# Kernel optimization log

Hardware: AMD Instinct MI355X
Metric: run time of the kernel (lower is better)

## Reference

```python
import jax, jax.numpy as jnp
import numpy as np
from jax import lax

B, T, D, NH = 8, 2048, 128, 4
HD = D // NH
EPS = 1e-5


def _ln(x, g, b):
    m = x.mean(-1, keepdims=True)
    v = ((x - m) ** 2).mean(-1, keepdims=True)
    return (x - m) / jnp.sqrt(v + EPS) * g + b


def _gelu(x):  # exact (erf) GELU, matching torch nn.GELU default
    return jax.nn.gelu(x, approximate=False)


def _forward(lob_feat, trade_feat, has_trade,
             ei_w, ei_b, ei_g, ei_beta, decay,
             in_proj_w, in_proj_b, out_proj_w, out_proj_b,
             cn_g, cn_b,
             lob_w, lob_b, lob_g, lob_beta,
             tr_w, tr_b, tr_g, tr_beta,
             of_w, of_b, of_g, of_beta):
    # event impact: Linear -> LayerNorm -> Tanh, gated by has_trade
    impact = jnp.tanh(_ln(trade_feat @ ei_w.T + ei_b, ei_g, ei_beta))
    impact = impact * has_trade[..., None]              # [B,T,D]

    # diagonal linear recurrence: state_t = sigmoid(decay) * state_{t-1} + impact_t
    d = jax.nn.sigmoid(decay)                           # [D]

    def step(s, x):
        s = d * s + x
        return s, s

    _, states = lax.scan(step, jnp.zeros_like(impact[:, 0]),
                         jnp.swapaxes(impact, 0, 1))    # [T,B,D]
    state_seq = jnp.swapaxes(states, 0, 1)              # [B,T,D]

    # fusion MLPs (dropout is identity in eval)
    lob_enh = _gelu(_ln(jnp.concatenate([lob_feat, state_seq], -1) @ lob_w.T + lob_b,
                        lob_g, lob_beta))
    trade_enh = _gelu(_ln(jnp.concatenate([trade_feat, state_seq], -1) @ tr_w.T + tr_b,
                          tr_g, tr_beta))

    # torch nn.MultiheadAttention (batch_first): q=lob_enh, k=v=trade_enh
    wq, wk, wv = in_proj_w[:D], in_proj_w[D:2 * D], in_proj_w[2 * D:]
    bq, bk, bv = in_proj_b[:D], in_proj_b[D:2 * D], in_proj_b[2 * D:]
    q = (lob_enh @ wq.T + bq).reshape(B, T, NH, HD)
    k = (trade_enh @ wk.T + bk).reshape(B, T, NH, HD)
    v = (trade_enh @ wv.T + bv).reshape(B, T, NH, HD)
    scores = jnp.einsum('bqhd,bkhd->bhqk', q, k) / jnp.sqrt(jnp.float32(HD))
    attn = jax.nn.softmax(scores, axis=-1)
    ctx = jnp.einsum('bhqk,bkhd->bqhd', attn, v).reshape(B, T, D)
    fused_attn = ctx @ out_proj_w.T + out_proj_b

    fused = _ln(lob_enh + fused_attn, cn_g, cn_b)
    output = _gelu(_ln(jnp.concatenate([fused, trade_enh], -1) @ of_w.T + of_b,
                       of_g, of_beta))
    return output


def setup_inputs() -> dict:
    key = jax.random.key(0)
    ks = jax.random.split(key, 20)
    s1 = 1.0 / np.sqrt(D)
    s2 = 1.0 / np.sqrt(2 * D)
    return {
        'lob_feat': jax.random.normal(ks[0], (B, T, D), jnp.float32),
        'trade_feat': jax.random.normal(ks[1], (B, T, D), jnp.float32),
        'has_trade': (jax.random.uniform(ks[2], (B, T)) < 0.5).astype(jnp.float32),
        'ei_w': jax.random.normal(ks[3], (D, D), jnp.float32) * s1,
        'ei_b': jnp.zeros((D,), jnp.float32),
        'ei_g': jnp.ones((D,), jnp.float32),
        'ei_beta': jnp.zeros((D,), jnp.float32),
        'decay': jnp.ones((D,), jnp.float32) * 0.9,
        'in_proj_w': jax.random.normal(ks[4], (3 * D, D), jnp.float32) * s1,
        'in_proj_b': jnp.zeros((3 * D,), jnp.float32),
        'out_proj_w': jax.random.normal(ks[5], (D, D), jnp.float32) * s1,
        'out_proj_b': jnp.zeros((D,), jnp.float32),
        'cn_g': jnp.ones((D,), jnp.float32),
        'cn_b': jnp.zeros((D,), jnp.float32),
        'lob_w': jax.random.normal(ks[6], (D, 2 * D), jnp.float32) * s2,
        'lob_b': jnp.zeros((D,), jnp.float32),
        'lob_g': jnp.ones((D,), jnp.float32),
        'lob_beta': jnp.zeros((D,), jnp.float32),
        'tr_w': jax.random.normal(ks[7], (D, 2 * D), jnp.float32) * s2,
        'tr_b': jnp.zeros((D,), jnp.float32),
        'tr_g': jnp.ones((D,), jnp.float32),
        'tr_beta': jnp.zeros((D,), jnp.float32),
        'of_w': jax.random.normal(ks[8], (D, 2 * D), jnp.float32) * s2,
        'of_b': jnp.zeros((D,), jnp.float32),
        'of_g': jnp.ones((D,), jnp.float32),
        'of_beta': jnp.zeros((D,), jnp.float32),
    }


def reference(lob_feat, trade_feat, has_trade,
              ei_w, ei_b, ei_g, ei_beta, decay,
              in_proj_w, in_proj_b, out_proj_w, out_proj_b,
              cn_g, cn_b,
              lob_w, lob_b, lob_g, lob_beta,
              tr_w, tr_b, tr_g, tr_beta,
              of_w, of_b, of_g, of_beta):
    return _forward(lob_feat, trade_feat, has_trade,
                    ei_w, ei_b, ei_g, ei_beta, decay,
                    in_proj_w, in_proj_b, out_proj_w, out_proj_b,
                    cn_g, cn_b,
                    lob_w, lob_b, lob_g, lob_beta,
                    tr_w, tr_b, tr_g, tr_beta,
                    of_w, of_b, of_g, of_beta)
```

## Files before the change

kernel.cpp:

```cpp
#include <hip/hip_runtime.h>
#include <math.h>


#define T_  2048

typedef short bf16x8 __attribute__((ext_vector_type(8)));
typedef float f32x4  __attribute__((ext_vector_type(4)));
typedef unsigned short ushort_t;

__device__ __forceinline__ float sigm(float x) { return 1.0f / (1.0f + __expf(-x)); }

__device__ __forceinline__ unsigned short f2bf(float x) {
    union { float f; unsigned u; } v; v.f = x;
    unsigned r = v.u + 0x7FFFu + ((v.u >> 16) & 1u);
    return (unsigned short)(r >> 16);
}
__device__ __forceinline__ float bf2f(ushort_t u) {
    union { unsigned u; float f; } v; v.u = ((unsigned)u) << 16; return v.f;
}
__device__ __forceinline__ unsigned cvtpk(float a, float b) {
    unsigned r;
    asm("v_cvt_pk_bf16_f32 %0, %1, %2" : "=v"(r) : "v"(a), "v"(b));
    return r;
}

__device__ __forceinline__ float gelu_f(float x) {
    const float e = exp2f(fmaf(0.044715f * x, x * x, x) * -2.3022083f);
    return x * __builtin_amdgcn_rcpf(1.0f + e);
}
__device__ __forceinline__ float tanh_f(float y) {
    const float e = exp2f(y * 2.8853900818f);
    return 1.0f - 2.0f * __builtin_amdgcn_rcpf(e + 1.0f);
}
#define MX3(a, b, c) fmaxf(fmaxf((a), (b)), (c))

__device__ __forceinline__ bf16x8 ld_f32_bf8(const float* p) {
    const float4 a = *(const float4*)p;
    const float4 b = *(const float4*)(p + 4);
    union { unsigned u[4]; bf16x8 v; } o;
    o.u[0] = cvtpk(a.x, a.y); o.u[1] = cvtpk(a.z, a.w);
    o.u[2] = cvtpk(b.x, b.y); o.u[3] = cvtpk(b.z, b.w);
    return o.v;
}

__global__ __launch_bounds__(256) void prep_w(
    const float* __restrict__ eiw, const float* __restrict__ ipw,
    const float* __restrict__ opw, const float* __restrict__ lobw,
    const float* __restrict__ trw, const float* __restrict__ ofw,
    ushort_t* __restrict__ pool)
{
    const size_t i8 = ((size_t)blockIdx.x * 256 + threadIdx.x) * 8;
    const float* src; size_t off;
    if      (i8 < 16384)  { src = eiw;  off = 0; }
    else if (i8 < 65536)  { src = ipw;  off = 16384; }
    else if (i8 < 81920)  { src = opw;  off = 65536; }
    else if (i8 < 114688) { src = lobw; off = 81920; }
    else if (i8 < 147456) { src = trw;  off = 114688; }
    else                  { src = ofw;  off = 147456; }
    *(bf16x8*)(pool + i8) = ld_f32_bf8(src + (i8 - off));
}

__global__ __launch_bounds__(512) void ei_scan(
    const float* __restrict__ trade, const ushort_t* __restrict__ Wb,
    const float* __restrict__ bias, const float* __restrict__ gamma,
    const float* __restrict__ beta, const float* __restrict__ extra,
    const float* __restrict__ decay,
    ushort_t* __restrict__ imp_out, float* __restrict__ ends)
{
    __shared__ ushort_t imp_t[64][132];
    __shared__ float red[64][2][2];
    const int tid = threadIdx.x, wid = tid >> 6, lane = tid & 63;
    const int c2 = lane & 15, g = lane >> 4;
    const int rowblk = wid >> 1, chf = wid & 1, cb0 = chf * 4;
    const int RB = blockIdx.x * 64;
    const int R0 = RB + rowblk * 16;

    f32x4 acc[4] = {};
#pragma unroll
    for (int ch = 0; ch < 4; ch++) {
        const bf16x8 a = ld_f32_bf8(trade + (size_t)(R0 + c2) * 128 + ch * 32 + g * 8);
#pragma unroll
        for (int j = 0; j < 4; j++) {
            const bf16x8 b = *(const bf16x8*)(Wb + (size_t)((cb0 + j) * 16 + c2) * 128 + ch * 32 + g * 8);
            acc[j] = __builtin_amdgcn_mfma_f32_16x16x32_bf16(a, b, acc[j], 0, 0, 0);
        }
    }
    float gm[4], bt[4];
#pragma unroll
    for (int j = 0; j < 4; j++) {
        const int col = (cb0 + j) * 16 + c2;
        const float bb = bias[col];
        gm[j] = gamma[col]; bt[j] = beta[col];
#pragma unroll
        for (int r = 0; r < 4; r++) acc[j][r] += bb;
    }
#pragma unroll
    for (int r = 0; r < 4; r++) {
        float s = 0.f, ss = 0.f;
#pragma unroll
        for (int j = 0; j < 4; j++) { const float v = acc[j][r]; s += v; ss = fmaf(v, v, ss); }
#pragma unroll
        for (int o = 8; o; o >>= 1) { s += __shfl_xor(s, o); ss += __shfl_xor(ss, o); }
        if (c2 == 0) {
            red[rowblk * 16 + 4 * g + r][chf][0] = s;
            red[rowblk * 16 + 4 * g + r][chf][1] = ss;
        }
    }
    __syncthreads();
#pragma unroll
    for (int r = 0; r < 4; r++) {
        const int lr = rowblk * 16 + 4 * g + r;
        const float S  = red[lr][0][0] + red[lr][1][0];
        const float SS = red[lr][0][1] + red[lr][1][1];
        const float mean = S * (1.0f / 128.0f);
        const float rstd = rsqrtf(fmaxf(SS * (1.0f / 128.0f) - mean * mean, 0.0f) + 1e-5f);
        const int R = RB + lr;
        const float ext = extra[R];
#pragma unroll
        for (int j = 0; j < 4; j++) {
            const int col = (cb0 + j) * 16 + c2;
            const float y = (acc[j][r] - mean) * rstd * gm[j] + bt[j];
            const ushort_t ib = f2bf(tanh_f(y) * ext);
            imp_out[(size_t)R * 128 + col] = ib;
            imp_t[lr][col] = ib;
        }
    }
    __syncthreads();
    if (tid < 128) {
        const int c = tid;
        const float d = sigm(decay[c]);
        float s = 0.0f;
#pragma unroll 4
        for (int tl = 0; tl < 64; tl++) s = fmaf(d, s, bf2f(imp_t[tl][c]));
        const int b = RB >> 11, ch64 = (RB & 2047) >> 6;
        ends[((size_t)b * 32 + ch64) * 128 + c] = s;
    }
}

__global__ __launch_bounds__(256) void enh_qkv(
    const float* __restrict__ lobf, const float* __restrict__ traf,
    const ushort_t* __restrict__ stab,
    const ushort_t* __restrict__ lobw, const ushort_t* __restrict__ trw,
    const ushort_t* __restrict__ ipw, const float* __restrict__ ipb,
    const float* __restrict__ lob_b, const float* __restrict__ lob_g,
    const float* __restrict__ lob_beta,
    const float* __restrict__ tr_b, const float* __restrict__ tr_g,
    const float* __restrict__ tr_beta,
    ushort_t* __restrict__ lobe_b, ushort_t* __restrict__ tre_bf,
    ushort_t* __restrict__ qo, ushort_t* __restrict__ ko, ushort_t* __restrict__ vo2)
{
    __shared__ ushort_t lob_t[32][136];
    __shared__ ushort_t tre_t[32][136];
    __shared__ ushort_t vls[128][36];
    __shared__ float red[32][2][4];
    const int tid = threadIdx.x, wid = tid >> 6, lane = tid & 63;
    const int c2 = lane & 15, g = lane >> 4;
    const int rowblk = wid >> 1, chf = wid & 1, cb0 = chf * 4;
    const int RB = blockIdx.x * 32;
    const int R0 = RB + rowblk * 16;

    f32x4 aL[4] = {}, aT[4] = {};
#pragma unroll
    for (int ch = 0; ch < 8; ch++) {
        const int kk = (ch & 3) * 32;
        bf16x8 xl, xt;
        if (ch < 4) {
            xl = ld_f32_bf8(lobf + (size_t)(R0 + c2) * 128 + kk + g * 8);
            xt = ld_f32_bf8(traf + (size_t)(R0 + c2) * 128 + kk + g * 8);
        } else {
            xl = *(const bf16x8*)(stab + (size_t)(R0 + c2) * 128 + kk + g * 8);
            xt = xl;
        }
#pragma unroll
        for (int j = 0; j < 4; j++) {
            const size_t wo = (size_t)((cb0 + j) * 16 + c2) * 256 + ch * 32 + g * 8;
            aL[j] = __builtin_amdgcn_mfma_f32_16x16x32_bf16(xl, *(const bf16x8*)(lobw + wo), aL[j], 0, 0, 0);
            aT[j] = __builtin_amdgcn_mfma_f32_16x16x32_bf16(xt, *(const bf16x8*)(trw + wo), aT[j], 0, 0, 0);
        }
    }
#pragma unroll
    for (int j = 0; j < 4; j++) {
        const int col = (cb0 + j) * 16 + c2;
        const float bL = lob_b[col], bT = tr_b[col];
#pragma unroll
        for (int r = 0; r < 4; r++) { aL[j][r] += bL; aT[j][r] += bT; }
    }
#pragma unroll
    for (int r = 0; r < 4; r++) {
        float sL = 0.f, ssL = 0.f, sT = 0.f, ssT = 0.f;
#pragma unroll
        for (int j = 0; j < 4; j++) {
            const float vL = aL[j][r], vT = aT[j][r];
            sL += vL; ssL = fmaf(vL, vL, ssL);
            sT += vT; ssT = fmaf(vT, vT, ssT);
        }
#pragma unroll
        for (int o = 8; o; o >>= 1) {
            sL += __shfl_xor(sL, o); ssL += __shfl_xor(ssL, o);
            sT += __shfl_xor(sT, o); ssT += __shfl_xor(ssT, o);
        }
        if (c2 == 0) {
            float* rd = red[rowblk * 16 + 4 * g + r][chf];
            rd[0] = sL; rd[1] = ssL; rd[2] = sT; rd[3] = ssT;
        }
    }
    __syncthreads();
#pragma unroll
    for (int r = 0; r < 4; r++) {
        const int lr = rowblk * 16 + 4 * g + r;
        const int R = RB + lr;
        const float SL  = red[lr][0][0] + red[lr][1][0];
        const float SSL = red[lr][0][1] + red[lr][1][1];
        const float ST  = red[lr][0][2] + red[lr][1][2];
        const float SST = red[lr][0][3] + red[lr][1][3];
        const float mL = SL * (1.0f / 128.0f), mT = ST * (1.0f / 128.0f);
        const float rL = rsqrtf(fmaxf(SSL * (1.0f / 128.0f) - mL * mL, 0.0f) + 1e-5f);
        const float rT = rsqrtf(fmaxf(SST * (1.0f / 128.0f) - mT * mT, 0.0f) + 1e-5f);
#pragma unroll
        for (int j = 0; j < 4; j++) {
            const int col = (cb0 + j) * 16 + c2;
            const float yL = gelu_f((aL[j][r] - mL) * rL * lob_g[col] + lob_beta[col]);
            const float yT = gelu_f((aT[j][r] - mT) * rT * tr_g[col] + tr_beta[col]);
            const ushort_t lb = f2bf(yL);
            lobe_b[(size_t)R * 128 + col] = lb;
            lob_t[lr][col] = lb;
            const ushort_t tb = f2bf(yT);
            tre_bf[(size_t)R * 128 + col] = tb;
            tre_t[lr][col] = tb;
        }
    }
    __syncthreads();

    const float qscale = 0.17677669529663687f * 1.4426950408889634f;
#pragma unroll
    for (int which = 0; which < 3; which++) {
        const ushort_t (*src)[136] = (which == 0) ? lob_t : tre_t;
        const ushort_t* Wp = ipw + (size_t)which * 16384;
        f32x4 pa[4] = {};
#pragma unroll
        for (int ch = 0; ch < 4; ch++) {
            const bf16x8 a = *(const bf16x8*)&src[rowblk * 16 + c2][ch * 32 + g * 8];
#pragma unroll
            for (int j = 0; j < 4; j++) {
                const bf16x8 b = *(const bf16x8*)(Wp + (size_t)((cb0 + j) * 16 + c2) * 128 + ch * 32 + g * 8);
                pa[j] = __builtin_amdgcn_mfma_f32_16x16x32_bf16(a, b, pa[j], 0, 0, 0);
            }
        }
        if (which < 2) {
            ushort_t* dst = (which == 0) ? qo : ko;
            const float sc = (which == 0) ? qscale : 1.0f;
#pragma unroll
            for (int j = 0; j < 4; j++) {
                const int col = (cb0 + j) * 16 + c2;
                const float bb = ipb[which * 128 + col];
                const int h = col >> 5, hd = col & 31;
#pragma unroll
                for (int r = 0; r < 4; r++) {
                    const int R = R0 + 4 * g + r;
                    const int b = R >> 11, t = R & 2047;
                    dst[(((size_t)b * 4 + h) * 2048 + t) * 32 + hd] = f2bf((pa[j][r] + bb) * sc);
                }
            }
        } else {
#pragma unroll
            for (int j = 0; j < 4; j++) {
                const int col = (cb0 + j) * 16 + c2;
                const float bb = ipb[256 + col];
#pragma unroll
                for (int r = 0; r < 4; r++)
                    vls[col][rowblk * 16 + 4 * g + r] = f2bf(pa[j][r] + bb);
            }
        }
    }
    __syncthreads();
    {
        const int col = tid >> 1, hf = tid & 1;
        const int h = col >> 5, hd = col & 31;
        const int nb = hd >> 4, c = hd & 15;
        const int b = RB >> 11;
        const int t0 = RB & 2047;
        const int kt = t0 >> 6, kh = (t0 >> 5) & 1;
        ushort_t* fbase = vo2 + ((size_t)(b * 4 + h)) * 65536 + kt * 2048 + kh * 1024 + nb * 512;
#pragma unroll
        for (int gp2 = 0; gp2 < 2; gp2++) {
            const int gp = 2 * hf + gp2;
            unsigned w[4];
#pragma unroll
            for (int e = 0; e < 4; e++) {
                const int p = gp * 8 + 2 * e;
                const int j2 = p & 7;
                const int lk = 4 * (p >> 3) + j2 + (j2 >= 4 ? 12 : 0);
                w[e] = (unsigned)vls[col][lk] | ((unsigned)vls[col][lk + 1] << 16);
            }
            *(uint4*)(fbase + gp * 128 + c * 8) = *(const uint4*)&w[0];
        }
    }
}

__global__ __launch_bounds__(256) void attn_kernel(
    const ushort_t* __restrict__ q, const ushort_t* __restrict__ k,
    const ushort_t* __restrict__ v2,
    ushort_t* __restrict__ part, float* __restrict__ rs_part,
    float* __restrict__ m_part)
{
    const int tid = threadIdx.x, wid = tid >> 6, lane = tid & 63;
    const int c = lane & 15, g = lane >> 4;
    const int half = blockIdx.x & 1, qt = blockIdx.x >> 1;
    const int bh = blockIdx.y, b = bh >> 2, h = bh & 3;
    const ushort_t* kb_ = k  + (size_t)bh * 65536 + (size_t)half * 32768;
    const ushort_t* vt_ = v2 + (size_t)bh * 65536 + (size_t)half * 32768;
    const int q0 = qt * 128 + wid * 32;

    const ushort_t* qbase = q + ((size_t)bh * 2048 + q0) * 32;
    const bf16x8 qf0 = *(const bf16x8*)(qbase + (size_t)c * 32 + g * 8);
    const bf16x8 qf1 = *(const bf16x8*)(qbase + (size_t)(16 + c) * 32 + g * 8);

    bf16x8 ones;
#pragma unroll
    for (int i = 0; i < 8; i++) ones[i] = (short)0x3F80;

    float m0 = 0.0f, m1 = 0.0f;
    f32x4 acc[2][2] = {};
    f32x4 racc[2] = {};

    for (int kt = 0; kt < 16; kt++) {
        f32x4 s0[4], s1[4];
        __builtin_amdgcn_s_setprio(1);
#pragma unroll
        for (int kb2 = 0; kb2 < 4; kb2++) {
            const bf16x8 kf = *(const bf16x8*)(kb_ + ((size_t)(kt * 64 + kb2 * 16 + c)) * 32 + g * 8);
            f32x4 z = {};
            s0[kb2] = __builtin_amdgcn_mfma_f32_16x16x32_bf16(kf, qf0, z, 0, 0, 0);
            s1[kb2] = __builtin_amdgcn_mfma_f32_16x16x32_bf16(kf, qf1, z, 0, 0, 0);
        }
        __builtin_amdgcn_s_setprio(0);

        const float t0 = MX3(s0[0][0], s0[0][1], s0[0][2]);
        const float t1 = MX3(s0[0][3], s0[1][0], s0[1][1]);
        const float t2 = MX3(s0[1][2], s0[1][3], s0[2][0]);
        const float t3 = MX3(s0[2][1], s0[2][2], s0[2][3]);
        const float t4 = MX3(s0[3][0], s0[3][1], s0[3][2]);
        const float u0 = MX3(s1[0][0], s1[0][1], s1[0][2]);
        const float u1 = MX3(s1[0][3], s1[1][0], s1[1][1]);
        const float u2 = MX3(s1[1][2], s1[1][3], s1[2][0]);
        const float u3 = MX3(s1[2][1], s1[2][2], s1[2][3]);
        const float u4 = MX3(s1[3][0], s1[3][1], s1[3][2]);
        const float lm = fmaxf(MX3(MX3(t0, t1, t2), MX3(t3, t4, s0[3][3]), u0),
                               MX3(MX3(u1, u2, u3), u4, s1[3][3]));
        if (__any(lm > 80.0f || m0 != 0.0f || m1 != 0.0f)) {
            float l0 = -1e30f, l1 = -1e30f;
#pragma unroll
            for (int kb2 = 0; kb2 < 4; kb2++)
#pragma unroll
                for (int r = 0; r < 4; r++) { l0 = fmaxf(l0, s0[kb2][r]); l1 = fmaxf(l1, s1[kb2][r]); }
            l0 = fmaxf(l0, __shfl_xor(l0, 16)); l0 = fmaxf(l0, __shfl_xor(l0, 32));
            l1 = fmaxf(l1, __shfl_xor(l1, 16)); l1 = fmaxf(l1, __shfl_xor(l1, 32));
            const float n0 = fmaxf(m0, l0), n1 = fmaxf(m1, l1);
            const float a0 = exp2f(m0 - n0), a1 = exp2f(m1 - n1);
#pragma unroll
            for (int nb = 0; nb < 2; nb++)
#pragma unroll
                for (int r = 0; r < 4; r++) { acc[0][nb][r] *= a0; acc[1][nb][r] *= a1; }
#pragma unroll
            for (int r = 0; r < 4; r++) { racc[0][r] *= a0; racc[1][r] *= a1; }
            m0 = n0; m1 = n1;
#pragma unroll
            for (int kb2 = 0; kb2 < 4; kb2++)
#pragma unroll
                for (int r = 0; r < 4; r++) {
                    s0[kb2][r] = exp2f(s0[kb2][r] - m0);
                    s1[kb2][r] = exp2f(s1[kb2][r] - m1);
                }
        } else {
#pragma unroll
            for (int kb2 = 0; kb2 < 4; kb2++)
#pragma unroll
                for (int r = 0; r < 4; r++) {
                    s0[kb2][r] = exp2f(s0[kb2][r]);
                    s1[kb2][r] = exp2f(s1[kb2][r]);
                }
        }

        union { unsigned u[4]; bf16x8 v; } p0a, p0b, p1a, p1b;
        p0a.u[0] = cvtpk(s0[0][0], s0[0][1]); p0a.u[1] = cvtpk(s0[0][2], s0[0][3]);
        p0a.u[2] = cvtpk(s0[1][0], s0[1][1]); p0a.u[3] = cvtpk(s0[1][2], s0[1][3]);
        p0b.u[0] = cvtpk(s0[2][0], s0[2][1]); p0b.u[1] = cvtpk(s0[2][2], s0[2][3]);
        p0b.u[2] = cvtpk(s0[3][0], s0[3][1]); p0b.u[3] = cvtpk(s0[3][2], s0[3][3]);
        p1a.u[0] = cvtpk(s1[0][0], s1[0][1]); p1a.u[1] = cvtpk(s1[0][2], s1[0][3]);
        p1a.u[2] = cvtpk(s1[1][0], s1[1][1]); p1a.u[3] = cvtpk(s1[1][2], s1[1][3]);
        p1b.u[0] = cvtpk(s1[2][0], s1[2][1]); p1b.u[1] = cvtpk(s1[2][2], s1[2][3]);
        p1b.u[2] = cvtpk(s1[3][0], s1[3][1]); p1b.u[3] = cvtpk(s1[3][2], s1[3][3]);

        const ushort_t* vtile = vt_ + (size_t)kt * 2048;
        __builtin_amdgcn_s_setprio(1);
#pragma unroll
        for (int nb = 0; nb < 2; nb++) {
            const bf16x8 vfA = *(const bf16x8*)(vtile + nb * 512 + lane * 8);
            const bf16x8 vfB = *(const bf16x8*)(vtile + 1024 + nb * 512 + lane * 8);
            acc[0][nb] = __builtin_amdgcn_mfma_f32_16x16x32_bf16(vfA, p0a.v, acc[0][nb], 0, 0, 0);
            acc[0][nb] = __builtin_amdgcn_mfma_f32_16x16x32_bf16(vfB, p0b.v, acc[0][nb], 0, 0, 0);
            acc[1][nb] = __builtin_amdgcn_mfma_f32_16x16x32_bf16(vfA, p1a.v, acc[1][nb], 0, 0, 0);
            acc[1][nb] = __builtin_amdgcn_mfma_f32_16x16x32_bf16(vfB, p1b.v, acc[1][nb], 0, 0, 0);
        }
        racc[0] = __builtin_amdgcn_mfma_f32_16x16x32_bf16(ones, p0a.v, racc[0], 0, 0, 0);
        racc[0] = __builtin_amdgcn_mfma_f32_16x16x32_bf16(ones, p0b.v, racc[0], 0, 0, 0);
        racc[1] = __builtin_amdgcn_mfma_f32_16x16x32_bf16(ones, p1a.v, racc[1], 0, 0, 0);
        racc[1] = __builtin_amdgcn_mfma_f32_16x16x32_bf16(ones, p1b.v, racc[1], 0, 0, 0);
        __builtin_amdgcn_s_setprio(0);
    }

    ushort_t* pb = part + (size_t)half * 2097152;
#pragma unroll
    for (int qf = 0; qf < 2; qf++) {
        const int qrow = q0 + qf * 16 + c;
        ushort_t* dst = pb + ((size_t)(b * 2048 + qrow)) * 128 + h * 32;
#pragma unroll
        for (int nb = 0; nb < 2; nb++) {
            uint2 wv;
            wv.x = cvtpk(acc[qf][nb][0], acc[qf][nb][1]);
            wv.y = cvtpk(acc[qf][nb][2], acc[qf][nb][3]);
            *(uint2*)(dst + nb * 16 + 4 * g) = wv;
        }
    }
    if (g == 0) {
        float* rsp = rs_part + (size_t)(half * 32 + bh) * 2048;
        float* mp  = m_part  + (size_t)(half * 32 + bh) * 2048;
        rsp[q0 + c]      = racc[0][0];
        rsp[q0 + 16 + c] = racc[1][0];
        mp[q0 + c]       = m0;
        mp[q0 + 16 + c]  = m1;
    }
}

__global__ __launch_bounds__(256) void out_fuse(
    const ushort_t* __restrict__ ctxA, const ushort_t* __restrict__ ctxB,
    const float* __restrict__ rs_part, const float* __restrict__ m_part,
    const ushort_t* __restrict__ treb,
    const ushort_t* __restrict__ opw, const float* __restrict__ opb,
    const float* __restrict__ cn_g, const float* __restrict__ cn_b,
    const ushort_t* __restrict__ ofw, const float* __restrict__ of_b,
    const float* __restrict__ of_g, const float* __restrict__ of_beta,
    const ushort_t* __restrict__ lobe_b, float* __restrict__ out)
{
    __shared__ ushort_t fus_t[32][136];
    __shared__ float red[32][2][2];
    const int tid = threadIdx.x, wid = tid >> 6, lane = tid & 63;
    const int c2 = lane & 15, g = lane >> 4;
    const int rowblk = wid >> 1, chf = wid & 1, cb0 = chf * 4;
    const int RB = blockIdx.x * 32;
    const int R0 = RB + rowblk * 16;

    const int rowA = R0 + c2;
    const int bb2 = rowA >> 11, tt = rowA & 2047;
    float fA[4], fB[4];
#pragma unroll
    for (int h = 0; h < 4; h++) {
        const int bh = bb2 * 4 + h;
        const float mA = m_part[(size_t)bh * 2048 + tt];
        const float mB = m_part[(size_t)(32 + bh) * 2048 + tt];
        const float rA = rs_part[(size_t)bh * 2048 + tt];
        const float rB = rs_part[(size_t)(32 + bh) * 2048 + tt];
        const float M = fmaxf(mA, mB);
        const float wA = exp2f(mA - M), wB = exp2f(mB - M);
        const float inv = __builtin_amdgcn_rcpf(fmaf(rA, wA, rB * wB));
        fA[h] = wA * inv; fB[h] = wB * inv;
    }

    f32x4 acc[4] = {};
#pragma unroll
    for (int ch = 0; ch < 4; ch++) {
        const bf16x8 aA = *(const bf16x8*)(ctxA + (size_t)rowA * 128 + ch * 32 + g * 8);
        const bf16x8 aB = *(const bf16x8*)(ctxB + (size_t)rowA * 128 + ch * 32 + g * 8);
        union { unsigned u[4]; bf16x8 v; } am;
#pragma unroll
        for (int i = 0; i < 4; i++) {
            const float e0 = bf2f((ushort_t)aA[2 * i]) * fA[ch] + bf2f((ushort_t)aB[2 * i]) * fB[ch];
            const float e1 = bf2f((ushort_t)aA[2 * i + 1]) * fA[ch] + bf2f((ushort_t)aB[2 * i + 1]) * fB[ch];
            am.u[i] = cvtpk(e0, e1);
        }
#pragma unroll
        for (int j = 0; j < 4; j++) {
            const bf16x8 b = *(const bf16x8*)(opw + (size_t)((cb0 + j) * 16 + c2) * 128 + ch * 32 + g * 8);
            acc[j] = __builtin_amdgcn_mfma_f32_16x16x32_bf16(am.v, b, acc[j], 0, 0, 0);
        }
    }
#pragma unroll
    for (int j = 0; j < 4; j++) {
        const int col = (cb0 + j) * 16 + c2;
        const float bb = opb[col];
#pragma unroll
        for (int r = 0; r < 4; r++)
            acc[j][r] += bb + bf2f(lobe_b[(size_t)(R0 + 4 * g + r) * 128 + col]);
    }
#pragma unroll
    for (int r = 0; r < 4; r++) {
        float s = 0.f, ss = 0.f;
#pragma unroll
        for (int j = 0; j < 4; j++) { const float v = acc[j][r]; s += v; ss = fmaf(v, v, ss); }
#pragma unroll
        for (int o = 8; o; o >>= 1) { s += __shfl_xor(s, o); ss += __shfl_xor(ss, o); }
        if (c2 == 0) {
            red[rowblk * 16 + 4 * g + r][chf][0] = s;
            red[rowblk * 16 + 4 * g + r][chf][1] = ss;
        }
    }
    __syncthreads();
#pragma unroll
    for (int r = 0; r < 4; r++) {
        const int lr = rowblk * 16 + 4 * g + r;
        const float S  = red[lr][0][0] + red[lr][1][0];
        const float SS = red[lr][0][1] + red[lr][1][1];
        const float mean = S * (1.0f / 128.0f);
        const float rstd = rsqrtf(fmaxf(SS * (1.0f / 128.0f) - mean * mean, 0.0f) + 1e-5f);
#pragma unroll
        for (int j = 0; j < 4; j++) {
            const int col = (cb0 + j) * 16 + c2;
            fus_t[lr][col] = f2bf((acc[j][r] - mean) * rstd * cn_g[col] + cn_b[col]);
        }
    }
    __syncthreads();

    f32x4 a2[4] = {};
#pragma unroll
    for (int ch = 0; ch < 8; ch++) {
        bf16x8 a;
        if (ch < 4) a = *(const bf16x8*)&fus_t[rowblk * 16 + c2][ch * 32 + g * 8];
        else        a = *(const bf16x8*)(treb + (size_t)(R0 + c2) * 128 + (ch - 4) * 32 + g * 8);
#pragma unroll
        for (int j = 0; j < 4; j++) {
            const bf16x8 b = *(const bf16x8*)(ofw + (size_t)((cb0 + j) * 16 + c2) * 256 + ch * 32 + g * 8);
            a2[j] = __builtin_amdgcn_mfma_f32_16x16x32_bf16(a, b, a2[j], 0, 0, 0);
        }
    }
#pragma unroll
    for (int j = 0; j < 4; j++) {
        const float bb = of_b[(cb0 + j) * 16 + c2];
#pragma unroll
        for (int r = 0; r < 4; r++) a2[j][r] += bb;
    }
#pragma unroll
    for (int r = 0; r < 4; r++) {
        float s = 0.f, ss = 0.f;
#pragma unroll
        for (int j = 0; j < 4; j++) { const float v = a2[j][r]; s += v; ss = fmaf(v, v, ss); }
#pragma unroll
        for (int o = 8; o; o >>= 1) { s += __shfl_xor(s, o); ss += __shfl_xor(ss, o); }
        if (c2 == 0) {
            red[rowblk * 16 + 4 * g + r][chf][0] = s;
            red[rowblk * 16 + 4 * g + r][chf][1] = ss;
        }
    }
    __syncthreads();
#pragma unroll
    for (int r = 0; r < 4; r++) {
        const int lr = rowblk * 16 + 4 * g + r;
        const float S  = red[lr][0][0] + red[lr][1][0];
        const float SS = red[lr][0][1] + red[lr][1][1];
        const float mean = S * (1.0f / 128.0f);
        const float rstd = rsqrtf(fmaxf(SS * (1.0f / 128.0f) - mean * mean, 0.0f) + 1e-5f);
        const int R = RB + lr;
#pragma unroll
        for (int j = 0; j < 4; j++) {
            const int col = (cb0 + j) * 16 + c2;
            const float y = (a2[j][r] - mean) * rstd * of_g[col] + of_beta[col];
            out[(size_t)R * 128 + col] = gelu_f(y);
        }
    }
}

__global__ void scan_carry_kernel(const float* __restrict__ ends,
                                  const float* __restrict__ decay,
                                  float* __restrict__ carry)
{
    const int c = threadIdx.x;
    const int b = blockIdx.x;
    const float d = sigm(decay[c]);
    float dl = d;
#pragma unroll
    for (int i = 0; i < 6; i++) dl *= dl;
    float e = 0.0f;
#pragma unroll
    for (int ch = 0; ch < 32; ch++) {
        carry[((size_t)b * 32 + ch) * 128 + c] = e;
        e = fmaf(dl, e, ends[((size_t)b * 32 + ch) * 128 + c]);
    }
}

__global__ void scan_fin_kernel(const ushort_t* __restrict__ imp,
                                const float* __restrict__ decay,
                                const float* __restrict__ carry,
                                ushort_t* __restrict__ stbf)
{
    const int c = threadIdx.x;
    const int ch = blockIdx.x, b = blockIdx.y;
    const float d = sigm(decay[c]);
    float s = carry[((size_t)b * 32 + ch) * 128 + c];
    const size_t base = ((size_t)b * T_ + ch * 64) * 128 + c;
#pragma unroll 4
    for (int tl = 0; tl < 64; tl++) {
        s = fmaf(d, s, bf2f(imp[base + (size_t)tl * 128]));
        stbf[base + (size_t)tl * 128] = f2bf(s);
    }
}

extern "C" void kernel_launch(void* const* d_in, const int* in_sizes, int n_in,
                              void* d_out, int out_size, void* d_ws, size_t ws_size,
                              hipStream_t stream)
{
    const float* lob_feat   = (const float*)d_in[0];
    const float* trade_feat = (const float*)d_in[1];
    const float* has_trade  = (const float*)d_in[2];
    const float* ei_w       = (const float*)d_in[3];
    const float* ei_b       = (const float*)d_in[4];
    const float* ei_g       = (const float*)d_in[5];
    const float* ei_beta    = (const float*)d_in[6];
    const float* decay      = (const float*)d_in[7];
    const float* in_proj_w  = (const float*)d_in[8];
    const float* in_proj_b  = (const float*)d_in[9];
    const float* out_proj_w = (const float*)d_in[10];
    const float* out_proj_b = (const float*)d_in[11];
    const float* cn_g       = (const float*)d_in[12];
    const float* cn_b       = (const float*)d_in[13];
    const float* lob_w      = (const float*)d_in[14];
    const float* lob_b      = (const float*)d_in[15];
    const float* lob_g      = (const float*)d_in[16];
    const float* lob_beta   = (const float*)d_in[17];
    const float* tr_w       = (const float*)d_in[18];
    const float* tr_b       = (const float*)d_in[19];
    const float* tr_g       = (const float*)d_in[20];
    const float* tr_beta    = (const float*)d_in[21];
    const float* of_w       = (const float*)d_in[22];
    const float* of_b       = (const float*)d_in[23];
    const float* of_g       = (const float*)d_in[24];
    const float* of_beta    = (const float*)d_in[25];

    char* W = (char*)d_ws;
    const size_t MB = 1u << 20;
    ushort_t* lobe_b   = (ushort_t*)W;
    ushort_t* state_bf = (ushort_t*)(W + 4 * MB);
    ushort_t* tre_bf   = (ushort_t*)(W + 8 * MB);
    ushort_t* q_bf     = (ushort_t*)(W + 12 * MB);
    ushort_t* k_bf     = (ushort_t*)(W + 16 * MB);
    ushort_t* v2       = (ushort_t*)(W + 20 * MB);
    ushort_t* pool     = (ushort_t*)(W + 24 * MB);
    float*    carry    = (float*)(W + 25 * MB);
    float*    ends     = (float*)(W + 25 * MB + 256 * 1024);
    ushort_t* imp_bf   = (ushort_t*)(W + 26 * MB);
    ushort_t* part     = (ushort_t*)(W + 30 * MB);
    float*    rs_part  = (float*)(W + 38 * MB);
    float*    m_part   = (float*)(W + 38 * MB + 512 * 1024);

    ushort_t* eiw_bf   = pool;
    ushort_t* ipw_bf   = pool + 16384;
    ushort_t* opw_bf   = pool + 65536;
    ushort_t* lobw_bf  = pool + 81920;
    ushort_t* trw_bf   = pool + 114688;
    ushort_t* ofw_bf   = pool + 147456;

    ushort_t* ctxA = part;
    ushort_t* ctxB = part + 2097152;

    const dim3 blk(256);

    prep_w<<<dim3(88), blk, 0, stream>>>(ei_w, in_proj_w, out_proj_w, lob_w, tr_w, of_w, pool);
    ei_scan<<<dim3(256), dim3(512), 0, stream>>>(trade_feat, eiw_bf, ei_b, ei_g, ei_beta,
                                                 has_trade, decay, imp_bf, ends);
    scan_carry_kernel<<<dim3(8), dim3(128), 0, stream>>>(ends, decay, carry);
    scan_fin_kernel<<<dim3(32, 8), dim3(128), 0, stream>>>(imp_bf, decay, carry, state_bf);
    enh_qkv<<<dim3(512), blk, 0, stream>>>(lob_feat, trade_feat, state_bf, lobw_bf, trw_bf,
                                           ipw_bf, in_proj_b, lob_b, lob_g, lob_beta,
                                           tr_b, tr_g, tr_beta, lobe_b, tre_bf,
                                           q_bf, k_bf, v2);
    attn_kernel<<<dim3(32, 32), blk, 0, stream>>>(q_bf, k_bf, v2, part, rs_part, m_part);
    out_fuse<<<dim3(512), blk, 0, stream>>>(ctxA, ctxB, rs_part, m_part, tre_bf,
                                            opw_bf, out_proj_b, cn_g, cn_b,
                                            ofw_bf, of_b, of_g, of_beta, lobe_b, (float*)d_out);
}
```

Baseline: 161.0 us.

## Stage K/V tiles in LDS with async double-buffering and four-way key split

The attention kernel now copies K and V tiles into double-buffered shared memory with asynchronous global-to-LDS loads, prefetching the next tile while the current one is computed. K is written in a pre-swizzled fragment layout by the QKV kernel so each lane reads its fragment directly. The key range is split into four partitions instead of two, doubling the grid, and the output kernel merges four partial softmax results. Row sums are accumulated with scalar adds instead of extra MFMAs against a ones matrix, and the two query fragments are processed one after the other to reduce register pressure under an occupancy launch bound. The trade-offs are more partial-result traffic to merge and a barrier on every tile.

```diff
diff --git a/kernel.cpp b/kernel.cpp
--- a/kernel.cpp
+++ b/kernel.cpp
@@ -7,6 +7,9 @@
 typedef short bf16x8 __attribute__((ext_vector_type(8)));
 typedef float f32x4  __attribute__((ext_vector_type(4)));
 typedef unsigned short ushort_t;
+
+#define GLOBAL_AS(p) ((const __attribute__((address_space(1))) unsigned int*)(p))
+#define LDS_AS(p)    ((__attribute__((address_space(3))) unsigned int*)(p))
 
 __device__ __forceinline__ float sigm(float x) { return 1.0f / (1.0f + __expf(-x)); }
 
@@ -246,19 +249,32 @@
                 pa[j] = __builtin_amdgcn_mfma_f32_16x16x32_bf16(a, b, pa[j], 0, 0, 0);
             }
         }
-        if (which < 2) {
-            ushort_t* dst = (which == 0) ? qo : ko;
-            const float sc = (which == 0) ? qscale : 1.0f;
+        if (which == 0) {
 #pragma unroll
             for (int j = 0; j < 4; j++) {
                 const int col = (cb0 + j) * 16 + c2;
-                const float bb = ipb[which * 128 + col];
+                const float bb = ipb[col];
                 const int h = col >> 5, hd = col & 31;
 #pragma unroll
                 for (int r = 0; r < 4; r++) {
                     const int R = R0 + 4 * g + r;
                     const int b = R >> 11, t = R & 2047;
-                    dst[(((size_t)b * 4 + h) * 2048 + t) * 32 + hd] = f2bf((pa[j][r] + bb) * sc);
+                    qo[(((size_t)b * 4 + h) * 2048 + t) * 32 + hd] = f2bf((pa[j][r] + bb) * qscale);
+                }
+            }
+        } else if (which == 1) {
+#pragma unroll
+            for (int j = 0; j < 4; j++) {
+                const int col = (cb0 + j) * 16 + c2;
+                const float bb = ipb[128 + col];
+                const int h = col >> 5, hd = col & 31;
+#pragma unroll
+                for (int r = 0; r < 4; r++) {
+                    const int R = R0 + 4 * g + r;
+                    const int b = R >> 11, t = R & 2047;
+                    ko[(size_t)(b * 4 + h) * 65536 + (size_t)(t >> 6) * 2048
+                       + (size_t)((t >> 4) & 3) * 512 + (hd >> 3) * 128 + (t & 15) * 8 + (hd & 7)]
+                        = f2bf(pa[j][r] + bb);
                 }
             }
         } else {
@@ -297,123 +313,171 @@
     }
 }
 
-__global__ __launch_bounds__(256) void attn_kernel(
-    const ushort_t* __restrict__ q, const ushort_t* __restrict__ k,
+__global__ __launch_bounds__(256, 8) void attn_kernel(
+    const ushort_t* __restrict__ q, const ushort_t* __restrict__ k2,
     const ushort_t* __restrict__ v2,
     ushort_t* __restrict__ part, float* __restrict__ rs_part,
     float* __restrict__ m_part)
 {
+    __shared__ ushort_t ks[2][2048];
+    __shared__ ushort_t vt[2][2048];
     const int tid = threadIdx.x, wid = tid >> 6, lane = tid & 63;
     const int c = lane & 15, g = lane >> 4;
-    const int half = blockIdx.x & 1, qt = blockIdx.x >> 1;
+    const int kq = blockIdx.x & 3, qt = blockIdx.x >> 2;
     const int bh = blockIdx.y, b = bh >> 2, h = bh & 3;
-    const ushort_t* kb_ = k  + (size_t)bh * 65536 + (size_t)half * 32768;
-    const ushort_t* vt_ = v2 + (size_t)bh * 65536 + (size_t)half * 32768;
+    const ushort_t* kt_base = k2 + (size_t)bh * 65536 + (size_t)kq * 16384;
+    const ushort_t* vt_base = v2 + (size_t)bh * 65536 + (size_t)kq * 16384;
     const int q0 = qt * 128 + wid * 32;
 
     const ushort_t* qbase = q + ((size_t)bh * 2048 + q0) * 32;
     const bf16x8 qf0 = *(const bf16x8*)(qbase + (size_t)c * 32 + g * 8);
     const bf16x8 qf1 = *(const bf16x8*)(qbase + (size_t)(16 + c) * 32 + g * 8);
 
-    bf16x8 ones;
-#pragma unroll
-    for (int i = 0; i < 8; i++) ones[i] = (short)0x3F80;
-
-    float m0 = 0.0f, m1 = 0.0f;
+    float m0 = 0.0f, m1 = 0.0f, rs0 = 0.0f, rs1 = 0.0f;
     f32x4 acc[2][2] = {};
-    f32x4 racc[2] = {};
-
-    for (int kt = 0; kt < 16; kt++) {
-        f32x4 s0[4], s1[4];
-        __builtin_amdgcn_s_setprio(1);
-#pragma unroll
-        for (int kb2 = 0; kb2 < 4; kb2++) {
-            const bf16x8 kf = *(const bf16x8*)(kb_ + ((size_t)(kt * 64 + kb2 * 16 + c)) * 32 + g * 8);
-            f32x4 z = {};
-            s0[kb2] = __builtin_amdgcn_mfma_f32_16x16x32_bf16(kf, qf0, z, 0, 0, 0);
-            s1[kb2] = __builtin_amdgcn_mfma_f32_16x16x32_bf16(kf, qf1, z, 0, 0, 0);
-        }
-        __builtin_amdgcn_s_setprio(0);
-
-        const float t0 = MX3(s0[0][0], s0[0][1], s0[0][2]);
-        const float t1 = MX3(s0[0][3], s0[1][0], s0[1][1]);
-        const float t2 = MX3(s0[1][2], s0[1][3], s0[2][0]);
-        const float t3 = MX3(s0[2][1], s0[2][2], s0[2][3]);
-        const float t4 = MX3(s0[3][0], s0[3][1], s0[3][2]);
-        const float u0 = MX3(s1[0][0], s1[0][1], s1[0][2]);
-        const float u1 = MX3(s1[0][3], s1[1][0], s1[1][1]);
-        const float u2 = MX3(s1[1][2], s1[1][3], s1[2][0]);
-        const float u3 = MX3(s1[2][1], s1[2][2], s1[2][3]);
-        const float u4 = MX3(s1[3][0], s1[3][1], s1[3][2]);
-        const float lm = fmaxf(MX3(MX3(t0, t1, t2), MX3(t3, t4, s0[3][3]), u0),
-                               MX3(MX3(u1, u2, u3), u4, s1[3][3]));
-        if (__any(lm > 80.0f || m0 != 0.0f || m1 != 0.0f)) {
-            float l0 = -1e30f, l1 = -1e30f;
-#pragma unroll
-            for (int kb2 = 0; kb2 < 4; kb2++)
-#pragma unroll
-                for (int r = 0; r < 4; r++) { l0 = fmaxf(l0, s0[kb2][r]); l1 = fmaxf(l1, s1[kb2][r]); }
-            l0 = fmaxf(l0, __shfl_xor(l0, 16)); l0 = fmaxf(l0, __shfl_xor(l0, 32));
-            l1 = fmaxf(l1, __shfl_xor(l1, 16)); l1 = fmaxf(l1, __shfl_xor(l1, 32));
-            const float n0 = fmaxf(m0, l0), n1 = fmaxf(m1, l1);
-            const float a0 = exp2f(m0 - n0), a1 = exp2f(m1 - n1);
-#pragma unroll
-            for (int nb = 0; nb < 2; nb++)
-#pragma unroll
-                for (int r = 0; r < 4; r++) { acc[0][nb][r] *= a0; acc[1][nb][r] *= a1; }
-#pragma unroll
-            for (int r = 0; r < 4; r++) { racc[0][r] *= a0; racc[1][r] *= a1; }
-            m0 = n0; m1 = n1;
-#pragma unroll
-            for (int kb2 = 0; kb2 < 4; kb2++)
-#pragma unroll
-                for (int r = 0; r < 4; r++) {
-                    s0[kb2][r] = exp2f(s0[kb2][r] - m0);
-                    s1[kb2][r] = exp2f(s1[kb2][r] - m1);
-                }
-        } else {
-#pragma unroll
-            for (int kb2 = 0; kb2 < 4; kb2++)
-#pragma unroll
-                for (int r = 0; r < 4; r++) {
-                    s0[kb2][r] = exp2f(s0[kb2][r]);
-                    s1[kb2][r] = exp2f(s1[kb2][r]);
-                }
-        }
-
-        union { unsigned u[4]; bf16x8 v; } p0a, p0b, p1a, p1b;
-        p0a.u[0] = cvtpk(s0[0][0], s0[0][1]); p0a.u[1] = cvtpk(s0[0][2], s0[0][3]);
-        p0a.u[2] = cvtpk(s0[1][0], s0[1][1]); p0a.u[3] = cvtpk(s0[1][2], s0[1][3]);
-        p0b.u[0] = cvtpk(s0[2][0], s0[2][1]); p0b.u[1] = cvtpk(s0[2][2], s0[2][3]);
-        p0b.u[2] = cvtpk(s0[3][0], s0[3][1]); p0b.u[3] = cvtpk(s0[3][2], s0[3][3]);
-        p1a.u[0] = cvtpk(s1[0][0], s1[0][1]); p1a.u[1] = cvtpk(s1[0][2], s1[0][3]);
-        p1a.u[2] = cvtpk(s1[1][0], s1[1][1]); p1a.u[3] = cvtpk(s1[1][2], s1[1][3]);
-        p1b.u[0] = cvtpk(s1[2][0], s1[2][1]); p1b.u[1] = cvtpk(s1[2][2], s1[2][3]);
-        p1b.u[2] = cvtpk(s1[3][0], s1[3][1]); p1b.u[3] = cvtpk(s1[3][2], s1[3][3]);
-
-        const ushort_t* vtile = vt_ + (size_t)kt * 2048;
-        __builtin_amdgcn_s_setprio(1);
-#pragma unroll
-        for (int nb = 0; nb < 2; nb++) {
-            const bf16x8 vfA = *(const bf16x8*)(vtile + nb * 512 + lane * 8);
-            const bf16x8 vfB = *(const bf16x8*)(vtile + 1024 + nb * 512 + lane * 8);
-            acc[0][nb] = __builtin_amdgcn_mfma_f32_16x16x32_bf16(vfA, p0a.v, acc[0][nb], 0, 0, 0);
-            acc[0][nb] = __builtin_amdgcn_mfma_f32_16x16x32_bf16(vfB, p0b.v, acc[0][nb], 0, 0, 0);
-            acc[1][nb] = __builtin_amdgcn_mfma_f32_16x16x32_bf16(vfA, p1a.v, acc[1][nb], 0, 0, 0);
-            acc[1][nb] = __builtin_amdgcn_mfma_f32_16x16x32_bf16(vfB, p1b.v, acc[1][nb], 0, 0, 0);
-        }
-        racc[0] = __builtin_amdgcn_mfma_f32_16x16x32_bf16(ones, p0a.v, racc[0], 0, 0, 0);
-        racc[0] = __builtin_amdgcn_mfma_f32_16x16x32_bf16(ones, p0b.v, racc[0], 0, 0, 0);
-        racc[1] = __builtin_amdgcn_mfma_f32_16x16x32_bf16(ones, p1a.v, racc[1], 0, 0, 0);
-        racc[1] = __builtin_amdgcn_mfma_f32_16x16x32_bf16(ones, p1b.v, racc[1], 0, 0, 0);
-        __builtin_amdgcn_s_setprio(0);
-    }
-
-    ushort_t* pb = part + (size_t)half * 2097152;
+
+    const int soff = wid * 512 + lane * 8;
+
+    __builtin_amdgcn_global_load_lds(GLOBAL_AS(kt_base + soff), LDS_AS(&ks[0][wid * 512]), 16, 0, 0);
+    __builtin_amdgcn_global_load_lds(GLOBAL_AS(vt_base + soff), LDS_AS(&vt[0][wid * 512]), 16, 0, 0);
+    __syncthreads();
+
+    for (int kt = 0; kt < 8; kt++) {
+        const int cur = kt & 1;
+        if (kt + 1 < 8) {
+            __builtin_amdgcn_global_load_lds(GLOBAL_AS(kt_base + (kt + 1) * 2048 + soff),
+                                             LDS_AS(&ks[cur ^ 1][wid * 512]), 16, 0, 0);
+            __builtin_amdgcn_global_load_lds(GLOBAL_AS(vt_base + (kt + 1) * 2048 + soff),
+                                             LDS_AS(&vt[cur ^ 1][wid * 512]), 16, 0, 0);
+        }
+
+        {
+            f32x4 s[4];
+            __builtin_amdgcn_s_setprio(1);
+#pragma unroll
+            for (int kb2 = 0; kb2 < 4; kb2++) {
+                const bf16x8 kf = *(const bf16x8*)&ks[cur][kb2 * 512 + lane * 8];
+                f32x4 z = {};
+                s[kb2] = __builtin_amdgcn_mfma_f32_16x16x32_bf16(kf, qf0, z, 0, 0, 0);
+            }
+            __builtin_amdgcn_s_setprio(0);
+            const float t0 = MX3(s[0][0], s[0][1], s[0][2]);
+            const float t1 = MX3(s[0][3], s[1][0], s[1][1]);
+            const float t2 = MX3(s[1][2], s[1][3], s[2][0]);
+            const float t3 = MX3(s[2][1], s[2][2], s[2][3]);
+            const float t4 = MX3(s[3][0], s[3][1], s[3][2]);
+            const float lm = fmaxf(MX3(t0, t1, t2), MX3(t3, t4, s[3][3]));
+            if (__any(lm > 80.0f || m0 != 0.0f)) {
+                float l = lm;
+                l = fmaxf(l, __shfl_xor(l, 16));
+                l = fmaxf(l, __shfl_xor(l, 32));
+                const float n = fmaxf(m0, l);
+                const float a = exp2f(m0 - n);
+#pragma unroll
+                for (int nb = 0; nb < 2; nb++)
+#pragma unroll
+                    for (int r = 0; r < 4; r++) acc[0][nb][r] *= a;
+                rs0 *= a;
+                m0 = n;
+#pragma unroll
+                for (int kb2 = 0; kb2 < 4; kb2++)
+#pragma unroll
+                    for (int r = 0; r < 4; r++) s[kb2][r] = exp2f(s[kb2][r] - m0);
+            } else {
+#pragma unroll
+                for (int kb2 = 0; kb2 < 4; kb2++)
+#pragma unroll
+                    for (int r = 0; r < 4; r++) s[kb2][r] = exp2f(s[kb2][r]);
+            }
+            rs0 += (((s[0][0] + s[0][1]) + (s[0][2] + s[0][3]))
+                  + ((s[1][0] + s[1][1]) + (s[1][2] + s[1][3])))
+                 + (((s[2][0] + s[2][1]) + (s[2][2] + s[2][3]))
+                  + ((s[3][0] + s[3][1]) + (s[3][2] + s[3][3])));
+            union { unsigned u[4]; bf16x8 v; } pa, pb;
+            pa.u[0] = cvtpk(s[0][0], s[0][1]); pa.u[1] = cvtpk(s[0][2], s[0][3]);
+            pa.u[2] = cvtpk(s[1][0], s[1][1]); pa.u[3] = cvtpk(s[1][2], s[1][3]);
+            pb.u[0] = cvtpk(s[2][0], s[2][1]); pb.u[1] = cvtpk(s[2][2], s[2][3]);
+            pb.u[2] = cvtpk(s[3][0], s[3][1]); pb.u[3] = cvtpk(s[3][2], s[3][3]);
+            __builtin_amdgcn_s_setprio(1);
+#pragma unroll
+            for (int nb = 0; nb < 2; nb++) {
+                const bf16x8 v0 = *(const bf16x8*)&vt[cur][nb * 512 + lane * 8];
+                const bf16x8 v1 = *(const bf16x8*)&vt[cur][1024 + nb * 512 + lane * 8];
+                acc[0][nb] = __builtin_amdgcn_mfma_f32_16x16x32_bf16(v0, pa.v, acc[0][nb], 0, 0, 0);
+                acc[0][nb] = __builtin_amdgcn_mfma_f32_16x16x32_bf16(v1, pb.v, acc[0][nb], 0, 0, 0);
+            }
+            __builtin_amdgcn_s_setprio(0);
+        }
+
+        {
+            f32x4 s[4];
+            __builtin_amdgcn_s_setprio(1);
+#pragma unroll
+            for (int kb2 = 0; kb2 < 4; kb2++) {
+                const bf16x8 kf = *(const bf16x8*)&ks[cur][kb2 * 512 + lane * 8];
+                f32x4 z = {};
+                s[kb2] = __builtin_amdgcn_mfma_f32_16x16x32_bf16(kf, qf1, z, 0, 0, 0);
+            }
+            __builtin_amdgcn_s_setprio(0);
+            const float t0 = MX3(s[0][0], s[0][1], s[0][2]);
+            const float t1 = MX3(s[0][3], s[1][0], s[1][1]);
+            const float t2 = MX3(s[1][2], s[1][3], s[2][0]);
+            const float t3 = MX3(s[2][1], s[2][2], s[2][3]);
+            const float t4 = MX3(s[3][0], s[3][1], s[3][2]);
+            const float lm = fmaxf(MX3(t0, t1, t2), MX3(t3, t4, s[3][3]));
+            if (__any(lm > 80.0f || m1 != 0.0f)) {
+                float l = lm;
+                l = fmaxf(l, __shfl_xor(l, 16));
+                l = fmaxf(l, __shfl_xor(l, 32));
+                const float n = fmaxf(m1, l);
+                const float a = exp2f(m1 - n);
+#pragma unroll
+                for (int nb = 0; nb < 2; nb++)
+#pragma unroll
+                    for (int r = 0; r < 4; r++) acc[1][nb][r] *= a;
+                rs1 *= a;
+                m1 = n;
+#pragma unroll
+                for (int kb2 = 0; kb2 < 4; kb2++)
+#pragma unroll
+                    for (int r = 0; r < 4; r++) s[kb2][r] = exp2f(s[kb2][r] - m1);
+            } else {
+#pragma unroll
+                for (int kb2 = 0; kb2 < 4; kb2++)
+#pragma unroll
+                    for (int r = 0; r < 4; r++) s[kb2][r] = exp2f(s[kb2][r]);
+            }
+            rs1 += (((s[0][0] + s[0][1]) + (s[0][2] + s[0][3]))
+                  + ((s[1][0] + s[1][1]) + (s[1][2] + s[1][3])))
+                 + (((s[2][0] + s[2][1]) + (s[2][2] + s[2][3]))
+                  + ((s[3][0] + s[3][1]) + (s[3][2] + s[3][3])));
+            union { unsigned u[4]; bf16x8 v; } pa, pb;
+            pa.u[0] = cvtpk(s[0][0], s[0][1]); pa.u[1] = cvtpk(s[0][2], s[0][3]);
+            pa.u[2] = cvtpk(s[1][0], s[1][1]); pa.u[3] = cvtpk(s[1][2], s[1][3]);
+            pb.u[0] = cvtpk(s[2][0], s[2][1]); pb.u[1] = cvtpk(s[2][2], s[2][3]);
+            pb.u[2] = cvtpk(s[3][0], s[3][1]); pb.u[3] = cvtpk(s[3][2], s[3][3]);
+            __builtin_amdgcn_s_setprio(1);
+#pragma unroll
+            for (int nb = 0; nb < 2; nb++) {
+                const bf16x8 v0 = *(const bf16x8*)&vt[cur][nb * 512 + lane * 8];
+                const bf16x8 v1 = *(const bf16x8*)&vt[cur][1024 + nb * 512 + lane * 8];
+                acc[1][nb] = __builtin_amdgcn_mfma_f32_16x16x32_bf16(v0, pa.v, acc[1][nb], 0, 0, 0);
+                acc[1][nb] = __builtin_amdgcn_mfma_f32_16x16x32_bf16(v1, pb.v, acc[1][nb], 0, 0, 0);
+            }
+            __builtin_amdgcn_s_setprio(0);
+        }
+
+        __syncthreads();
+    }
+
+    rs0 += __shfl_xor(rs0, 16); rs0 += __shfl_xor(rs0, 32);
+    rs1 += __shfl_xor(rs1, 16); rs1 += __shfl_xor(rs1, 32);
+
+    ushort_t* pb2 = part + (size_t)kq * 2097152;
 #pragma unroll
     for (int qf = 0; qf < 2; qf++) {
         const int qrow = q0 + qf * 16 + c;
-        ushort_t* dst = pb + ((size_t)(b * 2048 + qrow)) * 128 + h * 32;
+        ushort_t* dst = pb2 + ((size_t)(b * 2048 + qrow)) * 128 + h * 32;
 #pragma unroll
         for (int nb = 0; nb < 2; nb++) {
             uint2 wv;
@@ -423,17 +487,17 @@
         }
     }
     if (g == 0) {
-        float* rsp = rs_part + (size_t)(half * 32 + bh) * 2048;
-        float* mp  = m_part  + (size_t)(half * 32 + bh) * 2048;
-        rsp[q0 + c]      = racc[0][0];
-        rsp[q0 + 16 + c] = racc[1][0];
+        float* rsp = rs_part + (size_t)(kq * 32 + bh) * 2048;
+        float* mp  = m_part  + (size_t)(kq * 32 + bh) * 2048;
+        rsp[q0 + c]      = rs0;
+        rsp[q0 + 16 + c] = rs1;
         mp[q0 + c]       = m0;
         mp[q0 + 16 + c]  = m1;
     }
 }
 
 __global__ __launch_bounds__(256) void out_fuse(
-    const ushort_t* __restrict__ ctxA, const ushort_t* __restrict__ ctxB,
+    const ushort_t* __restrict__ part,
     const float* __restrict__ rs_part, const float* __restrict__ m_part,
     const ushort_t* __restrict__ treb,
     const ushort_t* __restrict__ opw, const float* __restrict__ opb,
@@ -452,30 +516,41 @@
 
     const int rowA = R0 + c2;
     const int bb2 = rowA >> 11, tt = rowA & 2047;
-    float fA[4], fB[4];
+    float f[4][4];
 #pragma unroll
     for (int h = 0; h < 4; h++) {
         const int bh = bb2 * 4 + h;
-        const float mA = m_part[(size_t)bh * 2048 + tt];
-        const float mB = m_part[(size_t)(32 + bh) * 2048 + tt];
-        const float rA = rs_part[(size_t)bh * 2048 + tt];
-        const float rB = rs_part[(size_t)(32 + bh) * 2048 + tt];
-        const float M = fmaxf(mA, mB);
-        const float wA = exp2f(mA - M), wB = exp2f(mB - M);
-        const float inv = __builtin_amdgcn_rcpf(fmaf(rA, wA, rB * wB));
-        fA[h] = wA * inv; fB[h] = wB * inv;
+        float m[4], r[4];
+#pragma unroll
+        for (int s = 0; s < 4; s++) {
+            m[s] = m_part[(size_t)(s * 32 + bh) * 2048 + tt];
+            r[s] = rs_part[(size_t)(s * 32 + bh) * 2048 + tt];
+        }
+        const float M = fmaxf(fmaxf(m[0], m[1]), fmaxf(m[2], m[3]));
+        float w[4], den = 0.f;
+#pragma unroll
+        for (int s = 0; s < 4; s++) { w[s] = exp2f(m[s] - M); den = fmaf(r[s], w[s], den); }
+        const float inv = __builtin_amdgcn_rcpf(den);
+#pragma unroll
+        for (int s = 0; s < 4; s++) f[s][h] = w[s] * inv;
     }
 
     f32x4 acc[4] = {};
 #pragma unroll
     for (int ch = 0; ch < 4; ch++) {
-        const bf16x8 aA = *(const bf16x8*)(ctxA + (size_t)rowA * 128 + ch * 32 + g * 8);
-        const bf16x8 aB = *(const bf16x8*)(ctxB + (size_t)rowA * 128 + ch * 32 + g * 8);
+        bf16x8 a[4];
+#pragma unroll
+        for (int s = 0; s < 4; s++)
+            a[s] = *(const bf16x8*)(part + (size_t)s * 2097152 + (size_t)rowA * 128 + ch * 32 + g * 8);
         union { unsigned u[4]; bf16x8 v; } am;
 #pragma unroll
         for (int i = 0; i < 4; i++) {
-            const float e0 = bf2f((ushort_t)aA[2 * i]) * fA[ch] + bf2f((ushort_t)aB[2 * i]) * fB[ch];
-            const float e1 = bf2f((ushort_t)aA[2 * i + 1]) * fA[ch] + bf2f((ushort_t)aB[2 * i + 1]) * fB[ch];
+            float e0 = 0.f, e1 = 0.f;
+#pragma unroll
+            for (int s = 0; s < 4; s++) {
+                e0 = fmaf(bf2f((ushort_t)a[s][2 * i]), f[s][ch], e0);
+                e1 = fmaf(bf2f((ushort_t)a[s][2 * i + 1]), f[s][ch], e1);
+            }
             am.u[i] = cvtpk(e0, e1);
         }
 #pragma unroll
@@ -640,15 +715,15 @@
     ushort_t* state_bf = (ushort_t*)(W + 4 * MB);
     ushort_t* tre_bf   = (ushort_t*)(W + 8 * MB);
     ushort_t* q_bf     = (ushort_t*)(W + 12 * MB);
-    ushort_t* k_bf     = (ushort_t*)(W + 16 * MB);
+    ushort_t* k2       = (ushort_t*)(W + 16 * MB);
     ushort_t* v2       = (ushort_t*)(W + 20 * MB);
     ushort_t* pool     = (ushort_t*)(W + 24 * MB);
     float*    carry    = (float*)(W + 25 * MB);
     float*    ends     = (float*)(W + 25 * MB + 256 * 1024);
     ushort_t* imp_bf   = (ushort_t*)(W + 26 * MB);
     ushort_t* part     = (ushort_t*)(W + 30 * MB);
-    float*    rs_part  = (float*)(W + 38 * MB);
-    float*    m_part   = (float*)(W + 38 * MB + 512 * 1024);
+    float*    rs_part  = (float*)(W + 46 * MB);
+    float*    m_part   = (float*)(W + 47 * MB);
 
     ushort_t* eiw_bf   = pool;
     ushort_t* ipw_bf   = pool + 16384;
@@ -656,9 +731,6 @@
     ushort_t* lobw_bf  = pool + 81920;
     ushort_t* trw_bf   = pool + 114688;
     ushort_t* ofw_bf   = pool + 147456;
-
-    ushort_t* ctxA = part;
-    ushort_t* ctxB = part + 2097152;
 
     const dim3 blk(256);
 
@@ -670,9 +742,9 @@
     enh_qkv<<<dim3(512), blk, 0, stream>>>(lob_feat, trade_feat, state_bf, lobw_bf, trw_bf,
                                            ipw_bf, in_proj_b, lob_b, lob_g, lob_beta,
                                            tr_b, tr_g, tr_beta, lobe_b, tre_bf,
-                                           q_bf, k_bf, v2);
-    attn_kernel<<<dim3(32, 32), blk, 0, stream>>>(q_bf, k_bf, v2, part, rs_part, m_part);
-    out_fuse<<<dim3(512), blk, 0, stream>>>(ctxA, ctxB, rs_part, m_part, tre_bf,
+                                           q_bf, k2, v2);
+    attn_kernel<<<dim3(64, 32), blk, 0, stream>>>(q_bf, k2, v2, part, rs_part, m_part);
+    out_fuse<<<dim3(512), blk, 0, stream>>>(part, rs_part, m_part, tre_bf,
                                             opw_bf, out_proj_b, cn_g, cn_b,
                                             ofw_bf, of_b, of_g, of_beta, lobe_b, (float*)d_out);
 }
```

Measured after the change: 234.1 us. 45.4% more time.
